# Kernel optimization log

Measured on AMD Instinct MI355X. Metric: run time of the kernel, lower is better.

## Reference

```python
import jax, jax.numpy as jnp
import numpy as np


def setup_inputs() -> dict:
    key = jax.random.key(0)
    k1, k2 = jax.random.split(key)
    B, N, C = 128, 200000, 100
    values = jax.random.normal(k1, (B, N), dtype=jnp.float32)
    labels = jax.random.randint(k2, (N,), 0, C, dtype=jnp.int64)
    return {"values": values, "labels": labels, "num_classes": C}


def reference(values, labels, num_classes):
    # Stratified (label-grouped) max pooling:
    # values: [B, N], labels: [N] in [0, num_classes)
    # output: [B, num_classes], out[b, c] = max over columns j with labels[j] == c
    # segment_max reduces over the leading axis, so operate on values.T [N, B].
    pooled = jax.ops.segment_max(
        values.T, labels, num_segments=num_classes, indices_are_sorted=False
    )  # [C, B]
    return pooled.T  # [B, C]
```

## Files before the change

### kernel.cpp

```cpp
#include <hip/hip_runtime.h>
#include <hip/hip_bf16.h>


#define TPBS 256
#define SMAX 16
#define ENC_NEG_INF 0x007FFFFFu

typedef float f4 __attribute__((ext_vector_type(4)));

__device__ __forceinline__ unsigned enc32(unsigned u) {
    return u ^ ((unsigned)(((int)u) >> 31) | 0x80000000u);
}
__device__ __forceinline__ float dec32(unsigned u) {
    unsigned b = u ^ (~(unsigned)(((int)u) >> 31) | 0x80000000u);
    return __uint_as_float(b);
}

__global__ __launch_bounds__(TPBS) void strat_lab8(
    const int* __restrict__ labels, unsigned char* __restrict__ l8, int N) {
    int i = blockIdx.x * TPBS + threadIdx.x;
    if (i < N) l8[i] = (unsigned char)labels[i];
}

__global__ __launch_bounds__(TPBS) void strat_stream(
    const float* __restrict__ values, const unsigned char* __restrict__ l8,
    unsigned* __restrict__ part, int B, int N, int C, int S, int SPAN, int CPAD) {
    extern __shared__ unsigned acc[];

    const int tid = threadIdx.x;
    const int blk = blockIdx.x;
    const int s   = blk % S;
    const int b   = blk / S;

    for (int i = tid; i < 4 * CPAD; i += TPBS) acc[i] = ENC_NEG_INF;
    __syncthreads();

    const int off0 = s * SPAN;
    const int len  = min(SPAN, N - off0);
    if (len > 0) {
        unsigned* qacc = acc + ((tid & 63) >> 4) * CPAD;
        const f4* vp = (const f4*)(values + (size_t)b * N + off0);
        const uchar4* lp = (const uchar4*)(l8 + off0);
        const int nv = len >> 2;

        for (int i = tid; i < nv; i += TPBS) {
            f4 v = __builtin_nontemporal_load(vp + i);
            uchar4 L = lp[i];
            unsigned e0 = enc32(__float_as_uint(v.x));
            unsigned e1 = enc32(__float_as_uint(v.y));
            unsigned e2 = enc32(__float_as_uint(v.z));
            unsigned e3 = enc32(__float_as_uint(v.w));
            if (e0 > qacc[L.x]) atomicMax(&qacc[L.x], e0);
            if (e1 > qacc[L.y]) atomicMax(&qacc[L.y], e1);
            if (e2 > qacc[L.z]) atomicMax(&qacc[L.z], e2);
            if (e3 > qacc[L.w]) atomicMax(&qacc[L.w], e3);
        }
        for (int j = (nv << 2) + tid; j < len; j += TPBS) {
            unsigned e = enc32(__float_as_uint(values[(size_t)b * N + off0 + j]));
            unsigned char c = l8[off0 + j];
            if (e > qacc[c]) atomicMax(&qacc[c], e);
        }
    }
    __syncthreads();

    unsigned* dst = part + (size_t)s * B * C + (size_t)b * C;
    for (int c = tid; c < C; c += TPBS) {
        unsigned m = max(max(acc[c], acc[CPAD + c]),
                         max(acc[2 * CPAD + c], acc[3 * CPAD + c]));
        dst[c] = m;
    }
}

__global__ __launch_bounds__(TPBS) void strat_red(
    const unsigned* __restrict__ part, float* __restrict__ out, int BC, int S) {
    const int i = blockIdx.x * TPBS + threadIdx.x;
    if (i >= BC) return;
    const unsigned* p = part + i;
    unsigned m0 = ENC_NEG_INF, m1 = ENC_NEG_INF, m2 = ENC_NEG_INF, m3 = ENC_NEG_INF;
    int s = 0;
    for (; s + 4 <= S; s += 4) {
        m0 = max(m0, p[(size_t)(s + 0) * BC]);
        m1 = max(m1, p[(size_t)(s + 1) * BC]);
        m2 = max(m2, p[(size_t)(s + 2) * BC]);
        m3 = max(m3, p[(size_t)(s + 3) * BC]);
    }
    for (; s < S; ++s) m0 = max(m0, p[(size_t)s * BC]);
    out[i] = dec32(max(max(m0, m1), max(m2, m3)));
}


#define TPB   256
#define ROWS  8
#define FCPAD 257

__device__ __forceinline__ unsigned encf(float f) {
    return enc32(__float_as_uint(f));
}

__global__ __launch_bounds__(TPB) void strat_init(unsigned* __restrict__ out_enc, int n) {
    int i = blockIdx.x * TPB + threadIdx.x;
    if (i < n) out_enc[i] = ENC_NEG_INF;
}

__global__ __launch_bounds__(TPB) void strat_main_atomic(
    const float* __restrict__ values, const int* __restrict__ labels,
    unsigned* __restrict__ out_enc, int B, int N, int C, int T) {
    __shared__ unsigned acc[ROWS * FCPAD];
    const int tid  = threadIdx.x;
    const int row0 = blockIdx.y * ROWS;
    const int rmax = min(ROWS, B - row0);

    for (int i = tid; i < ROWS * FCPAD; i += TPB) acc[i] = ENC_NEG_INF;
    __syncthreads();

    const int t = blockIdx.x;
#pragma unroll
    for (int e = 0; e < 4; ++e) {
        const int j = t * 1024 + tid * 4 + e;
        if (j < N) {
            const int c = labels[j];
            for (int r = 0; r < rmax; ++r)
                atomicMax(&acc[r * FCPAD + c],
                          encf(values[(size_t)(row0 + r) * N + j]));
        }
    }
    __syncthreads();
    for (int i = tid; i < rmax * C; i += TPB) {
        const int r = i / C, c = i - r * C;
        atomicMax(&out_enc[(size_t)(row0 + r) * C + c], acc[r * FCPAD + c]);
    }
}

__global__ __launch_bounds__(TPB) void strat_decode(unsigned* __restrict__ buf, int n) {
    int i = blockIdx.x * TPB + threadIdx.x;
    if (i < n) {
        float f = dec32(buf[i]);
        ((float*)buf)[i] = f;
    }
}


extern "C" void kernel_launch(void* const* d_in, const int* in_sizes, int n_in,
                              void* d_out, int out_size, void* d_ws, size_t ws_size,
                              hipStream_t stream) {
    const float* values = (const float*)d_in[0];
    const int*   labels = (const int*)d_in[1];
    const int N  = in_sizes[1];
    const int B  = in_sizes[0] / N;
    const int C  = out_size / B;
    const int BC = B * C;

    const int S    = SMAX;
    const int SPAN = (((N + S - 1) / S) + 3) & ~3;
    const int CPAD = ((C + 31) / 32) * 32 + 1;

    const size_t part_off   = ((size_t)N + 255) & ~(size_t)255;
    const size_t part_bytes = (size_t)S * BC * sizeof(unsigned);
    const size_t lds        = (size_t)4 * CPAD * sizeof(unsigned);

    const bool main_ok = (C <= 128) && (part_off + part_bytes <= ws_size) &&
                         ((size_t)S * SPAN >= (size_t)N);

    if (main_ok) {
        unsigned char* l8   = (unsigned char*)d_ws;
        unsigned*      part = (unsigned*)((char*)d_ws + part_off);

        strat_lab8<<<(N + TPBS - 1) / TPBS, TPBS, 0, stream>>>(labels, l8, N);

        strat_stream<<<S * B, TPBS, lds, stream>>>(
            values, l8, part, B, N, C, S, SPAN, CPAD);

        strat_red<<<(BC + TPBS - 1) / TPBS, TPBS, 0, stream>>>(
            part, (float*)d_out, BC, S);
    } else {
        unsigned* out_enc = (unsigned*)d_out;
        const int init_blocks = (out_size + TPB - 1) / TPB;
        strat_init<<<init_blocks, TPB, 0, stream>>>(out_enc, out_size);
        dim3 grid((N + 1023) / 1024, (B + ROWS - 1) / ROWS);
        strat_main_atomic<<<grid, TPB, 0, stream>>>(values, labels, out_enc, B, N, C,
                                                    (N + 1023) / 1024);
        strat_decode<<<init_blocks, TPB, 0, stream>>>(out_enc, out_size);
    }
}
```

Before: 146.9 us.

## Drop byte-label precompute kernel and unconditional LDS atomics with int32 labels

Removes the separate kernel that narrowed labels to uint8 and instead reads the int32 labels directly as int4 vectors in the streaming kernel. The check-before-atomicMax guard on the LDS accumulators is also removed, so every element issues an LDS atomic. This saves one kernel launch and a pass over the labels, but each of the 128 row blocks now reads four times more label bytes, and LDS atomic traffic rises because no compare-and-skip filters updates.

```diff
diff --git a/kernel.cpp b/kernel.cpp
--- a/kernel.cpp
+++ b/kernel.cpp
@@ -16,14 +16,8 @@
     return __uint_as_float(b);
 }
 
-__global__ __launch_bounds__(TPBS) void strat_lab8(
-    const int* __restrict__ labels, unsigned char* __restrict__ l8, int N) {
-    int i = blockIdx.x * TPBS + threadIdx.x;
-    if (i < N) l8[i] = (unsigned char)labels[i];
-}
-
 __global__ __launch_bounds__(TPBS) void strat_stream(
-    const float* __restrict__ values, const unsigned char* __restrict__ l8,
+    const float* __restrict__ values, const int* __restrict__ labels,
     unsigned* __restrict__ part, int B, int N, int C, int S, int SPAN, int CPAD) {
     extern __shared__ unsigned acc[];
 
@@ -40,25 +34,20 @@
     if (len > 0) {
         unsigned* qacc = acc + ((tid & 63) >> 4) * CPAD;
         const f4* vp = (const f4*)(values + (size_t)b * N + off0);
-        const uchar4* lp = (const uchar4*)(l8 + off0);
+        const int4* lp = (const int4*)(labels + off0);
         const int nv = len >> 2;
 
         for (int i = tid; i < nv; i += TPBS) {
             f4 v = __builtin_nontemporal_load(vp + i);
-            uchar4 L = lp[i];
-            unsigned e0 = enc32(__float_as_uint(v.x));
-            unsigned e1 = enc32(__float_as_uint(v.y));
-            unsigned e2 = enc32(__float_as_uint(v.z));
-            unsigned e3 = enc32(__float_as_uint(v.w));
-            if (e0 > qacc[L.x]) atomicMax(&qacc[L.x], e0);
-            if (e1 > qacc[L.y]) atomicMax(&qacc[L.y], e1);
-            if (e2 > qacc[L.z]) atomicMax(&qacc[L.z], e2);
-            if (e3 > qacc[L.w]) atomicMax(&qacc[L.w], e3);
+            int4 L = lp[i];
+            atomicMax(&qacc[L.x], enc32(__float_as_uint(v.x)));
+            atomicMax(&qacc[L.y], enc32(__float_as_uint(v.y)));
+            atomicMax(&qacc[L.z], enc32(__float_as_uint(v.z)));
+            atomicMax(&qacc[L.w], enc32(__float_as_uint(v.w)));
         }
         for (int j = (nv << 2) + tid; j < len; j += TPBS) {
-            unsigned e = enc32(__float_as_uint(values[(size_t)b * N + off0 + j]));
-            unsigned char c = l8[off0 + j];
-            if (e > qacc[c]) atomicMax(&qacc[c], e);
+            atomicMax(&qacc[labels[off0 + j]],
+                      enc32(__float_as_uint(values[(size_t)b * N + off0 + j])));
         }
     }
     __syncthreads();
@@ -154,21 +143,17 @@
     const int SPAN = (((N + S - 1) / S) + 3) & ~3;
     const int CPAD = ((C + 31) / 32) * 32 + 1;
 
-    const size_t part_off   = ((size_t)N + 255) & ~(size_t)255;
     const size_t part_bytes = (size_t)S * BC * sizeof(unsigned);
     const size_t lds        = (size_t)4 * CPAD * sizeof(unsigned);
 
-    const bool main_ok = (C <= 128) && (part_off + part_bytes <= ws_size) &&
+    const bool main_ok = (C <= 128) && (part_bytes <= ws_size) &&
                          ((size_t)S * SPAN >= (size_t)N);
 
     if (main_ok) {
-        unsigned char* l8   = (unsigned char*)d_ws;
-        unsigned*      part = (unsigned*)((char*)d_ws + part_off);
-
-        strat_lab8<<<(N + TPBS - 1) / TPBS, TPBS, 0, stream>>>(labels, l8, N);
+        unsigned* part = (unsigned*)d_ws;
 
         strat_stream<<<S * B, TPBS, lds, stream>>>(
-            values, l8, part, B, N, C, S, SPAN, CPAD);
+            values, labels, part, B, N, C, S, SPAN, CPAD);
 
         strat_red<<<(BC + TPBS - 1) / TPBS, TPBS, 0, stream>>>(
             part, (float*)d_out, BC, S);
```

New measurement: 150.3 us. 2.3% more time.
